# Kernel optimization log

Hardware: AMD Instinct MI355X
Metric: run time of the kernel (lower is better)

## Reference

```python
import jax, jax.numpy as jnp
import numpy as np

N = 50000      # num nodes
E = 1_600_000  # num edges (avg degree 32)
L = 200_000    # num label edges to decode
D_IN, H1, H2 = 256, 128, 64


def setup_inputs() -> dict:
    key = jax.random.key(0)
    ks = jax.random.split(key, 20)

    def w(k, fan_in, fan_out):
        return jax.random.normal(k, (fan_in, fan_out), jnp.float32) * (1.0 / np.sqrt(fan_in))

    return {
        'x': jax.random.normal(ks[0], (N, D_IN), jnp.float32),
        'prev0': jax.random.normal(ks[1], (N, H1), jnp.float32),
        'prev1': jax.random.normal(ks[2], (N, H2), jnp.float32),
        'Wpre1': w(ks[3], D_IN, 256), 'bpre1': jnp.zeros((256,), jnp.float32),
        'Wpre2': w(ks[4], 256, 128),  'bpre2': jnp.zeros((128,), jnp.float32),
        'Wc1': w(ks[5], 128, H1),     'bc1': jnp.zeros((H1,), jnp.float32),
        'Wc2': w(ks[6], H1, H2),      'bc2': jnp.zeros((H2,), jnp.float32),
        'Wm1': w(ks[7], 2 * H1, H1),  'bm1': jnp.zeros((H1,), jnp.float32),
        'Wm2': w(ks[8], 2 * H2, H2),  'bm2': jnp.zeros((H2,), jnp.float32),
        'Wpost': w(ks[9], H2, 2),     'bpost': jnp.zeros((2,), jnp.float32),
        'edge_index': jax.random.randint(ks[10], (2, E), 0, N, jnp.int32),
        'edge_label_index': jax.random.randint(ks[11], (2, L), 0, N, jnp.int32),
    }


def _gcn_conv(h, W, b, src, dst, n):
    """PyG GCNConv: add self-loops, sym-normalize D^-1/2 (A+I) D^-1/2 (X W) + b."""
    hw = h @ W                                   # [N, out]
    deg = jax.ops.segment_sum(jnp.ones_like(src, jnp.float32), dst, num_segments=n) + 1.0
    dinv = jax.lax.rsqrt(deg)                    # [N]
    norm = dinv[src] * dinv[dst]                 # [E]
    agg = jax.ops.segment_sum(hw[src] * norm[:, None], dst, num_segments=n)
    agg = agg + hw * (dinv * dinv)[:, None]      # self-loop term
    return agg + b


def reference(x, prev0, prev1, Wpre1, bpre1, Wpre2, bpre2, Wc1, bc1, Wc2, bc2,
              Wm1, bm1, Wm2, bm2, Wpost, bpost, edge_index, edge_label_index):
    # isnap > 0 with update='mlp'; dropout p=0.0 -> identity
    src, dst = edge_index[0], edge_index[1]
    n = x.shape[0]

    h = jax.nn.relu(x @ Wpre1 + bpre1)
    h = jax.nn.relu(h @ Wpre2 + bpre2)

    h = jax.nn.relu(_gcn_conv(h, Wc1, bc1, src, dst, n))
    h = jnp.concatenate([h, prev0], axis=1) @ Wm1 + bm1   # temporal MLP update 1
    emb0 = h

    h = jax.nn.relu(_gcn_conv(h, Wc2, bc2, src, dst, n))
    h = jnp.concatenate([h, prev1], axis=1) @ Wm2 + bm2   # temporal MLP update 2
    emb1 = h

    # hadamard edge decode
    h_had = emb1[edge_label_index[0]] * emb1[edge_label_index[1]]  # [L, H2]
    pred = jnp.sum(h_had @ Wpost + bpost, axis=-1)                 # [L]
    return pred, emb0, emb1
```

## Files before the change

### kernel.cpp

```cpp
#include <hip/hip_runtime.h>
#include <hip/hip_bf16.h>


typedef unsigned short ushort_t;
typedef __attribute__((ext_vector_type(8))) short s8v;
typedef __attribute__((ext_vector_type(4))) float f4;

#define BSHIFT 8

__device__ __forceinline__ ushort_t f2bf(float v) {
    unsigned u = __float_as_uint(v);
    return (ushort_t)((u + 0x7FFFu + ((u >> 16) & 1u)) >> 16);
}

__device__ __forceinline__ s8v cvt8(f4 v0, f4 v1) {
    ushort_t hb[8];
    hb[0] = f2bf(v0.x); hb[1] = f2bf(v0.y); hb[2] = f2bf(v0.z); hb[3] = f2bf(v0.w);
    hb[4] = f2bf(v1.x); hb[5] = f2bf(v1.y); hb[6] = f2bf(v1.z); hb[7] = f2bf(v1.w);
    return *(s8v*)hb;
}

__device__ __forceinline__ size_t swzidx(int row, int k, int Wd) {
    int p = (((k & 63) >> 3) ^ (row & 7));
    return (size_t)row * Wd + (k & ~63) + p * 8 + (k & 7);
}

__device__ __forceinline__ void dma16(const ushort_t* g, ushort_t* l) {
    __builtin_amdgcn_global_load_lds(
        (const __attribute__((address_space(1))) unsigned int*)g,
        (__attribute__((address_space(3))) unsigned int*)l, 16, 0, 0);
}

template <int W>
__global__ __launch_bounds__(256) void f2bswz_kernel(const float* __restrict__ in,
                                                     ushort_t* __restrict__ out, size_t n) {
    size_t i = ((size_t)blockIdx.x * 256 + threadIdx.x) * 8;
    if (i + 8 > n) return;
    f4 v0 = *(const f4*)&in[i];
    f4 v1 = *(const f4*)&in[i + 4];
    int row = (int)(i / W), k = (int)(i % W);
    *(s8v*)&out[swzidx(row, k, W)] = cvt8(v0, v1);
}

template <int BN, int KW, int K1, bool A1F32, bool RELU, bool SCALE, bool DUAL,
          int OUTMODE, bool SWZO>
__global__ __launch_bounds__(256, 2) void gemm_lds(
    const float* __restrict__ A1f, const ushort_t* __restrict__ A1h,
    const ushort_t* __restrict__ A2h,
    const ushort_t* __restrict__ Wt,
    const float* __restrict__ bias, const float* __restrict__ rowscale,
    float* __restrict__ Cf, ushort_t* __restrict__ Ch,
    int M, int Nout)
{
    constexpr int NT = BN / 32;
    constexpr int K2 = KW - K1;
    constexpr int NTILE = KW / 64;
    __shared__ ushort_t Abuf[2][128 * 64];
    __shared__ ushort_t Bbuf[2][BN * 64];

    const int tid  = threadIdx.x;
    const int lane = tid & 63;
    const int w    = tid >> 6;
    const int wr   = w >> 1, wc = w & 1;
    const int rbase = blockIdx.y * 128;
    const int bn    = blockIdx.x * BN;

    f4 acc[4][NT];
    const f4 zero = {0.f, 0.f, 0.f, 0.f};
#pragma unroll
    for (int mi = 0; mi < 4; ++mi)
#pragma unroll
        for (int ni = 0; ni < NT; ++ni) acc[mi][ni] = zero;

    f4 pr[8];

    auto gloadF32 = [&](int kt) {
#pragma unroll
        for (int j = 0; j < 4; ++j) {
            const int c2 = tid + j * 256;
            const int row = c2 >> 3, c = c2 & 7;
            const int gr = min(rbase + row, M - 1);
            const float* p = &A1f[(size_t)gr * K1 + kt + c * 8];
            pr[2 * j] = *(const f4*)p;
            pr[2 * j + 1] = *(const f4*)(p + 4);
        }
    };
    auto dswriteF32 = [&](int buf) {
#pragma unroll
        for (int j = 0; j < 4; ++j) {
            const int c2 = tid + j * 256;
            const int row = c2 >> 3, c = c2 & 7;
            const int pc = c ^ (row & 7);
            *(s8v*)&Abuf[buf][row * 64 + pc * 8] = cvt8(pr[2 * j], pr[2 * j + 1]);
        }
    };
    auto stageA = [&](int buf, int kt) {
#pragma unroll
        for (int i = 0; i < 4; ++i) {
            const int s = w * 4 + i;
            const int row = s * 8 + (lane >> 3);
            const int c = lane & 7;
            const int gr = min(rbase + row, M - 1);
            const ushort_t* g;
            if (DUAL && kt >= K1) g = &A2h[(size_t)gr * K2 + (kt - K1) + c * 8];
            else                  g = &A1h[(size_t)gr * K1 + kt + c * 8];
            dma16(g, &Abuf[buf][s * 512]);
        }
    };
    auto stageB = [&](int buf, int kt) {
#pragma unroll
        for (int i = 0; i < NT; ++i) {
            const int s = w * NT + i;
            const int colr = s * 8 + (lane >> 3);
            const int c = lane & 7;
            dma16(&Wt[(size_t)(bn + colr) * KW + kt + c * 8], &Bbuf[buf][s * 512]);
        }
    };

    if constexpr (A1F32) { gloadF32(0); dswriteF32(0); }
    else                 { stageA(0, 0); }
    stageB(0, 0);
    __syncthreads();

    for (int t = 0; t < NTILE; ++t) {
        const int cur = t & 1;
        if (t + 1 < NTILE) {
            if constexpr (A1F32) gloadF32((t + 1) * 64);
            else                 stageA(cur ^ 1, (t + 1) * 64);
            stageB(cur ^ 1, (t + 1) * 64);
        }
#pragma unroll
        for (int ks = 0; ks < 2; ++ks) {
            const int c = ks * 4 + (lane >> 4);
            s8v bfrag[NT];
#pragma unroll
            for (int ni = 0; ni < NT; ++ni) {
                const int colr = wc * (NT * 16) + ni * 16 + (lane & 15);
                bfrag[ni] = *(const s8v*)&Bbuf[cur][colr * 64 + (c ^ (colr & 7)) * 8];
            }
#pragma unroll
            for (int mi = 0; mi < 4; ++mi) {
                const int row = wr * 64 + mi * 16 + (lane & 15);
                const s8v af = *(const s8v*)&Abuf[cur][row * 64 + (c ^ (row & 7)) * 8];
#pragma unroll
                for (int ni = 0; ni < NT; ++ni)
                    acc[mi][ni] = __builtin_amdgcn_mfma_f32_16x16x32_bf16(af, bfrag[ni], acc[mi][ni], 0, 0, 0);
            }
        }
        if constexpr (A1F32) { if (t + 1 < NTILE) dswriteF32(cur ^ 1); }
        __syncthreads();
    }

#pragma unroll
    for (int mi = 0; mi < 4; ++mi) {
#pragma unroll
        for (int reg = 0; reg < 4; ++reg) {
            const int row = rbase + wr * 64 + mi * 16 + (lane >> 4) * 4 + reg;
            if (row >= M) continue;
            const float rs = SCALE ? rowscale[row] : 1.f;
#pragma unroll
            for (int ni = 0; ni < NT; ++ni) {
                const int col = bn + wc * (NT * 16) + ni * 16 + (lane & 15);
                float v = acc[mi][ni][reg];
                if (SCALE) v *= rs;
                if (bias) v += bias[col];
                if (RELU) v = fmaxf(v, 0.f);
                const size_t oidx = SWZO ? swzidx(row, col, Nout) : ((size_t)row * Nout + col);
                if constexpr (OUTMODE == 2) {
                    Ch[oidx] = f2bf(v);
                } else if constexpr (OUTMODE == 3) {
                    Cf[(size_t)row * Nout + col] = v;
                    Ch[oidx] = f2bf(v);
                } else {
                    Cf[(size_t)row * Nout + col] = v;
                }
            }
        }
    }
}

struct WDesc { const float* W; ushort_t* h; int K; int No; };
struct WAll { WDesc d[6]; };

__global__ void wtcvt_kernel(WAll wa) {
    WDesc d = wa.d[blockIdx.y];
    int e = blockIdx.x * blockDim.x + threadIdx.x;
    if (e >= d.K * d.No) return;
    int k = e / d.No, n = e - k * d.No;
    d.h[swzidx(n, k, d.K)] = f2bf(d.W[e]);
}

__global__ __launch_bounds__(256) void bcount_kernel(const int* __restrict__ dst,
                                                     int* __restrict__ bcount, int E, int NB) {
    __shared__ int cnt[256];
    const int t = threadIdx.x;
    if (t < NB) cnt[t] = 0;
    __syncthreads();
    for (int e = blockIdx.x * 256 + t; e < E; e += gridDim.x * 256)
        atomicAdd(&cnt[dst[e] >> BSHIFT], 1);
    __syncthreads();
    if (t < NB && cnt[t]) atomicAdd(&bcount[t], cnt[t]);
}

__global__ __launch_bounds__(256) void bscan_kernel(const int* __restrict__ bcount,
                                                    int* __restrict__ bbase,
                                                    int* __restrict__ bcursor, int NB, int E) {
    __shared__ int s[256];
    const int t = threadIdx.x;
    s[t] = (t < NB) ? bcount[t] : 0;
    __syncthreads();
    for (int off = 1; off < 256; off <<= 1) {
        int v = (t >= off) ? s[t - off] : 0;
        __syncthreads();
        s[t] += v;
        __syncthreads();
    }
    int excl = t ? s[t - 1] : 0;
    if (t < NB) { bbase[t] = excl; bcursor[t] = excl; }
    if (t == 0) bbase[NB] = E;
}

__global__ __launch_bounds__(256) void bpart_kernel(const int* __restrict__ src,
                                                    const int* __restrict__ dst,
                                                    int* __restrict__ bcursor,
                                                    unsigned* __restrict__ packed, int E, int NB) {
    __shared__ int cnt[256];
    __shared__ int cur[256];
    const int t = threadIdx.x;
    const int beg = blockIdx.x * 8192;
    const int end = min(beg + 8192, E);
    if (t < NB) cnt[t] = 0;
    __syncthreads();
    for (int e = beg + t; e < end; e += 256) atomicAdd(&cnt[dst[e] >> BSHIFT], 1);
    __syncthreads();
    if (t < NB && cnt[t]) cur[t] = atomicAdd(&bcursor[t], cnt[t]);
    __syncthreads();
    for (int e = beg + t; e < end; e += 256) {
        int d = dst[e];
        int b = d >> BSHIFT;
        int pos = atomicAdd(&cur[b], 1);
        packed[pos] = (unsigned)src[e] | ((unsigned)(d & ((1 << BSHIFT) - 1)) << 16);
    }
}

__global__ __launch_bounds__(256) void bbuild_kernel(const int* __restrict__ bbase,
                                                     const unsigned* __restrict__ packed,
                                                     int* __restrict__ col,
                                                     int* __restrict__ rowstart,
                                                     float* __restrict__ dinv, int N, int E) {
    __shared__ int ncnt[256];
    __shared__ int s[256];
    __shared__ int ncur[256];
    const int b = blockIdx.x;
    const int t = threadIdx.x;
    const int beg = bbase[b], end = bbase[b + 1];
    const int node0 = b << BSHIFT;
    const int nInB = min(256, N - node0);
    ncnt[t] = 0;
    __syncthreads();
    for (int e = beg + t; e < end; e += 256) atomicAdd(&ncnt[packed[e] >> 16], 1);
    __syncthreads();
    s[t] = ncnt[t];
    __syncthreads();
    for (int off = 1; off < 256; off <<= 1) {
        int v = (t >= off) ? s[t - off] : 0;
        __syncthreads();
        s[t] += v;
        __syncthreads();
    }
    int excl = t ? s[t - 1] : 0;
    if (t < nInB) {
        rowstart[node0 + t] = beg + excl;
        dinv[node0 + t] = rsqrtf((float)ncnt[t] + 1.0f);
    }
    ncur[t] = beg + excl;
    __syncthreads();
    for (int e = beg + t; e < end; e += 256) {
        unsigned p = packed[e];
        int pos = atomicAdd(&ncur[p >> 16], 1);
        col[pos] = (int)(p & 0xFFFFu);
    }
    if (b == 0 && t == 0) rowstart[N] = E;
}

template <int F>
__global__ __launch_bounds__(256) void gather_bf_kernel(const int* __restrict__ rowstart,
                                                        const int* __restrict__ col,
                                                        const float* __restrict__ dinv,
                                                        const ushort_t* __restrict__ hws,
                                                        const float* __restrict__ bias,
                                                        ushort_t* __restrict__ aggb, int N) {
    const int wave = threadIdx.x >> 6;
    const int lane = threadIdx.x & 63;
    const int d = blockIdx.x * 4 + wave;
    if (d >= N) return;
    const int beg = rowstart[d], end = rowstart[d + 1];
    const float dd = dinv[d];
    if (F == 128) {
        const unsigned* base = (const unsigned*)hws;
        unsigned sv = base[(size_t)d * 64 + lane];
        float ax = __uint_as_float(sv << 16);
        float ay = __uint_as_float(sv & 0xFFFF0000u);
        for (int e0 = beg; e0 < end; e0 += 64) {
            int nid = (e0 + lane < end) ? col[e0 + lane] : 0;
            int cnt = min(64, end - e0);
            int j = 0;
            for (; j + 8 <= cnt; j += 8) {
                unsigned u[8];
#pragma unroll
                for (int q = 0; q < 8; ++q) {
                    int s = __shfl(nid, j + q);
                    u[q] = base[(size_t)s * 64 + lane];
                }
#pragma unroll
                for (int q = 0; q < 8; ++q) {
                    ax += __uint_as_float(u[q] << 16);
                    ay += __uint_as_float(u[q] & 0xFFFF0000u);
                }
            }
            for (; j < cnt; ++j) {
                int s = __shfl(nid, j);
                unsigned uu = base[(size_t)s * 64 + lane];
                ax += __uint_as_float(uu << 16);
                ay += __uint_as_float(uu & 0xFFFF0000u);
            }
        }
        float2 b = ((const float2*)bias)[lane];
        float rx = fmaxf(ax * dd + b.x, 0.f);
        float ry = fmaxf(ay * dd + b.y, 0.f);
        unsigned pk = ((unsigned)f2bf(ry) << 16) | (unsigned)f2bf(rx);
        const int p = ((lane >> 2) & 7) ^ (d & 7);
        const int uidx = (lane >> 5) * 32 + p * 4 + (lane & 3);
        ((unsigned*)aggb)[(size_t)d * 64 + uidx] = pk;
    } else {
        float acc = __uint_as_float((unsigned)hws[(size_t)d * 64 + lane] << 16);
        for (int e0 = beg; e0 < end; e0 += 64) {
            int nid = (e0 + lane < end) ? col[e0 + lane] : 0;
            int cnt = min(64, end - e0);
            int j = 0;
            for (; j + 8 <= cnt; j += 8) {
                ushort_t u[8];
#pragma unroll
                for (int q = 0; q < 8; ++q) {
                    int s = __shfl(nid, j + q);
                    u[q] = hws[(size_t)s * 64 + lane];
                }
#pragma unroll
                for (int q = 0; q < 8; ++q) acc += __uint_as_float((unsigned)u[q] << 16);
            }
            for (; j < cnt; ++j) {
                int s = __shfl(nid, j);
                acc += __uint_as_float((unsigned)hws[(size_t)s * 64 + lane] << 16);
            }
        }
        acc = fmaxf(acc * dd + bias[lane], 0.f);
        const int p = (lane >> 3) ^ (d & 7);
        aggb[(size_t)d * 64 + p * 8 + (lane & 7)] = f2bf(acc);
    }
}

__global__ __launch_bounds__(256) void decode_kernel(const ushort_t* __restrict__ emb1b,
                                                     const int* __restrict__ eli,
                                                     const float* __restrict__ Wpost,
                                                     const float* __restrict__ bpost,
                                                     float* __restrict__ pred, int L) {
    const int wave = threadIdx.x >> 6;
    const int lane = threadIdx.x & 63;
    const int l = blockIdx.x * 4 + wave;
    if (l >= L) return;
    int s = eli[l];
    int d = eli[L + l];
    float w = Wpost[lane * 2] + Wpost[lane * 2 + 1];
    float a = __uint_as_float((unsigned)emb1b[(size_t)s * 64 + lane] << 16);
    float b = __uint_as_float((unsigned)emb1b[(size_t)d * 64 + lane] << 16);
    float p = a * b * w;
#pragma unroll
    for (int off = 32; off; off >>= 1) p += __shfl_down(p, off);
    if (lane == 0) pred[l] = p + bpost[0] + bpost[1];
}

extern "C" void kernel_launch(void* const* d_in, const int* in_sizes, int n_in,
                              void* d_out, int out_size, void* d_ws, size_t ws_size,
                              hipStream_t stream) {
    const float* x     = (const float*)d_in[0];
    const float* prev0 = (const float*)d_in[1];
    const float* prev1 = (const float*)d_in[2];
    const float* Wpre1 = (const float*)d_in[3];
    const float* bpre1 = (const float*)d_in[4];
    const float* Wpre2 = (const float*)d_in[5];
    const float* bpre2 = (const float*)d_in[6];
    const float* Wc1   = (const float*)d_in[7];
    const float* bc1   = (const float*)d_in[8];
    const float* Wc2   = (const float*)d_in[9];
    const float* bc2   = (const float*)d_in[10];
    const float* Wm1   = (const float*)d_in[11];
    const float* bm1   = (const float*)d_in[12];
    const float* Wm2   = (const float*)d_in[13];
    const float* bm2   = (const float*)d_in[14];
    const float* Wpost = (const float*)d_in[15];
    const float* bpost = (const float*)d_in[16];
    const int* edge_index = (const int*)d_in[17];
    const int* eli        = (const int*)d_in[18];

    const int N = in_sizes[0] / 256;
    const int E = in_sizes[17] / 2;
    const int L = in_sizes[18] / 2;
    const int NB = (N + 255) >> BSHIFT;

    const int* src = edge_index;
    const int* dst = edge_index + E;

    float* out  = (float*)d_out;
    float* pred = out;
    float* emb0 = out + L;
    float* emb1 = out + L + (size_t)N * 128;

    float* ws = (float*)d_ws;
    unsigned* packed = (unsigned*)ws;
    ushort_t* h1h   = (ushort_t*)ws;
    ushort_t* hws1b = (ushort_t*)ws;
    ushort_t* emb0b = (ushort_t*)ws;
    ushort_t* emb1b = (ushort_t*)ws;
    ushort_t* agg1b = (ushort_t*)(ws + (size_t)64 * N);
    ushort_t* hws2b = (ushort_t*)(ws + (size_t)64 * N);
    ushort_t* agg2b = (ushort_t*)(ws + (size_t)96 * N);
    ushort_t* h2b   = (ushort_t*)(ws + (size_t)128 * N);
    ushort_t* p0b   = (ushort_t*)(ws + (size_t)192 * N);
    ushort_t* p1b   = (ushort_t*)(ws + (size_t)256 * N);
    int*      col   = (int*)(ws + (size_t)288 * N);

    size_t o = (size_t)320 * N;
    int* rowstart = (int*)(ws + o);         o += ((size_t)N + 4) & ~(size_t)3;
    float* dinv = ws + o;                   o += ((size_t)N + 3) & ~(size_t)3;
    int* bbase = (int*)(ws + o);            o += 260;
    int* bcursor = (int*)(ws + o);          o += 260;
    int* bcount = (int*)(ws + o);           o += 260;
    ushort_t* wb = (ushort_t*)(ws + o);

    ushort_t* wpre1t = wb + 0;
    ushort_t* wpre2t = wb + 65536;
    ushort_t* wc1t   = wb + 98304;
    ushort_t* wm1t   = wb + 114688;
    ushort_t* wc2t   = wb + 147456;
    ushort_t* wm2t   = wb + 155648;

    {
        size_t n0 = (size_t)N * 128, n1 = (size_t)N * 64;
        f2bswz_kernel<128><<<(int)((n0 / 8 + 255) / 256), 256, 0, stream>>>(prev0, p0b, n0);
        f2bswz_kernel<64><<<(int)((n1 / 8 + 255) / 256), 256, 0, stream>>>(prev1, p1b, n1);
    }

    hipMemsetAsync(bcount, 0, (size_t)NB * sizeof(int), stream);
    bcount_kernel<<<1024, 256, 0, stream>>>(dst, bcount, E, NB);
    bscan_kernel<<<1, 256, 0, stream>>>(bcount, bbase, bcursor, NB, E);
    bpart_kernel<<<(E + 8191) / 8192, 256, 0, stream>>>(src, dst, bcursor, packed, E, NB);
    bbuild_kernel<<<NB, 256, 0, stream>>>(bbase, packed, col, rowstart, dinv, N, E);

    WAll wa;
    wa.d[0] = {Wpre1, wpre1t, 256, 256};
    wa.d[1] = {Wpre2, wpre2t, 256, 128};
    wa.d[2] = {Wc1,   wc1t,   128, 128};
    wa.d[3] = {Wm1,   wm1t,   256, 128};
    wa.d[4] = {Wc2,   wc2t,   128, 64};
    wa.d[5] = {Wm2,   wm2t,   128, 64};
    wtcvt_kernel<<<dim3(256, 6), 256, 0, stream>>>(wa);

    const int gy = (N + 127) / 128;

    gemm_lds<128, 256, 256, true, true, false, false, 2, true><<<dim3(2, gy), 256, 0, stream>>>(
        x, nullptr, nullptr, wpre1t, bpre1, nullptr, nullptr, h1h, N, 256);
    gemm_lds<128, 256, 256, false, true, false, false, 2, true><<<dim3(1, gy), 256, 0, stream>>>(
        nullptr, h1h, nullptr, wpre2t, bpre2, nullptr, nullptr, h2b, N, 128);
    gemm_lds<128, 128, 128, false, false, true, false, 2, false><<<dim3(1, gy), 256, 0, stream>>>(
        nullptr, h2b, nullptr, wc1t, nullptr, dinv, nullptr, hws1b, N, 128);
    gather_bf_kernel<128><<<(N + 3) / 4, 256, 0, stream>>>(rowstart, col, dinv, hws1b, bc1, agg1b, N);
    gemm_lds<128, 256, 128, false, false, false, true, 3, true><<<dim3(1, gy), 256, 0, stream>>>(
        nullptr, agg1b, p0b, wm1t, bm1, nullptr, emb0, emb0b, N, 128);
    gemm_lds<64, 128, 128, false, false, true, false, 2, false><<<dim3(1, gy), 256, 0, stream>>>(
        nullptr, emb0b, nullptr, wc2t, nullptr, dinv, nullptr, hws2b, N, 64);
    gather_bf_kernel<64><<<(N + 3) / 4, 256, 0, stream>>>(rowstart, col, dinv, hws2b, bc2, agg2b, N);
    gemm_lds<64, 128, 64, false, false, false, true, 3, false><<<dim3(1, gy), 256, 0, stream>>>(
        nullptr, agg2b, p1b, wm2t, bm2, nullptr, emb1, emb1b, N, 64);
    decode_kernel<<<(L + 3) / 4, 256, 0, stream>>>(emb1b, eli, Wpost, bpost, pred, L);
}
```

Before: 342.8 us.

## Replace double-buffered LDS pipeline with single-buffer load-sync-compute loop in GEMM

Removes double buffering and prefetch of the next K tile in the LDS GEMM. Each iteration now loads one A and B tile into a single shared buffer, syncs, computes, and syncs again. This halves LDS usage and register pressure, which may allow more resident blocks, but it stops global loads from overlapping with MFMA compute.

```diff
diff --git a/kernel.cpp b/kernel.cpp
--- a/kernel.cpp
+++ b/kernel.cpp
@@ -54,9 +54,8 @@
 {
     constexpr int NT = BN / 32;
     constexpr int K2 = KW - K1;
-    constexpr int NTILE = KW / 64;
-    __shared__ ushort_t Abuf[2][128 * 64];
-    __shared__ ushort_t Bbuf[2][BN * 64];
+    __shared__ ushort_t Abuf[128 * 64];
+    __shared__ ushort_t Bbuf[BN * 64];
 
     const int tid  = threadIdx.x;
     const int lane = tid & 63;
@@ -72,63 +71,38 @@
 #pragma unroll
         for (int ni = 0; ni < NT; ++ni) acc[mi][ni] = zero;
 
-    f4 pr[8];
-
-    auto gloadF32 = [&](int kt) {
-#pragma unroll
-        for (int j = 0; j < 4; ++j) {
-            const int c2 = tid + j * 256;
-            const int row = c2 >> 3, c = c2 & 7;
-            const int gr = min(rbase + row, M - 1);
-            const float* p = &A1f[(size_t)gr * K1 + kt + c * 8];
-            pr[2 * j] = *(const f4*)p;
-            pr[2 * j + 1] = *(const f4*)(p + 4);
-        }
-    };
-    auto dswriteF32 = [&](int buf) {
-#pragma unroll
-        for (int j = 0; j < 4; ++j) {
-            const int c2 = tid + j * 256;
-            const int row = c2 >> 3, c = c2 & 7;
-            const int pc = c ^ (row & 7);
-            *(s8v*)&Abuf[buf][row * 64 + pc * 8] = cvt8(pr[2 * j], pr[2 * j + 1]);
-        }
-    };
-    auto stageA = [&](int buf, int kt) {
-#pragma unroll
-        for (int i = 0; i < 4; ++i) {
-            const int s = w * 4 + i;
-            const int row = s * 8 + (lane >> 3);
-            const int c = lane & 7;
-            const int gr = min(rbase + row, M - 1);
-            const ushort_t* g;
-            if (DUAL && kt >= K1) g = &A2h[(size_t)gr * K2 + (kt - K1) + c * 8];
-            else                  g = &A1h[(size_t)gr * K1 + kt + c * 8];
-            dma16(g, &Abuf[buf][s * 512]);
-        }
-    };
-    auto stageB = [&](int buf, int kt) {
+    for (int kt = 0; kt < KW; kt += 64) {
+        if constexpr (A1F32) {
+#pragma unroll
+            for (int j = 0; j < 4; ++j) {
+                const int c2 = tid + j * 256;
+                const int row = c2 >> 3, c = c2 & 7;
+                const int gr = min(rbase + row, M - 1);
+                const float* p = &A1f[(size_t)gr * K1 + kt + c * 8];
+                const int pc = c ^ (row & 7);
+                *(s8v*)&Abuf[row * 64 + pc * 8] = cvt8(*(const f4*)p, *(const f4*)(p + 4));
+            }
+        } else {
+#pragma unroll
+            for (int i = 0; i < 4; ++i) {
+                const int s = w * 4 + i;
+                const int row = s * 8 + (lane >> 3);
+                const int c = lane & 7;
+                const int gr = min(rbase + row, M - 1);
+                const ushort_t* g;
+                if (DUAL && kt >= K1) g = &A2h[(size_t)gr * K2 + (kt - K1) + c * 8];
+                else                  g = &A1h[(size_t)gr * K1 + kt + c * 8];
+                dma16(g, &Abuf[s * 512]);
+            }
+        }
 #pragma unroll
         for (int i = 0; i < NT; ++i) {
             const int s = w * NT + i;
             const int colr = s * 8 + (lane >> 3);
             const int c = lane & 7;
-            dma16(&Wt[(size_t)(bn + colr) * KW + kt + c * 8], &Bbuf[buf][s * 512]);
-        }
-    };
-
-    if constexpr (A1F32) { gloadF32(0); dswriteF32(0); }
-    else                 { stageA(0, 0); }
-    stageB(0, 0);
-    __syncthreads();
-
-    for (int t = 0; t < NTILE; ++t) {
-        const int cur = t & 1;
-        if (t + 1 < NTILE) {
-            if constexpr (A1F32) gloadF32((t + 1) * 64);
-            else                 stageA(cur ^ 1, (t + 1) * 64);
-            stageB(cur ^ 1, (t + 1) * 64);
-        }
+            dma16(&Wt[(size_t)(bn + colr) * KW + kt + c * 8], &Bbuf[s * 512]);
+        }
+        __syncthreads();
 #pragma unroll
         for (int ks = 0; ks < 2; ++ks) {
             const int c = ks * 4 + (lane >> 4);
@@ -136,18 +110,17 @@
 #pragma unroll
             for (int ni = 0; ni < NT; ++ni) {
                 const int colr = wc * (NT * 16) + ni * 16 + (lane & 15);
-                bfrag[ni] = *(const s8v*)&Bbuf[cur][colr * 64 + (c ^ (colr & 7)) * 8];
+                bfrag[ni] = *(const s8v*)&Bbuf[colr * 64 + (c ^ (colr & 7)) * 8];
             }
 #pragma unroll
             for (int mi = 0; mi < 4; ++mi) {
                 const int row = wr * 64 + mi * 16 + (lane & 15);
-                const s8v af = *(const s8v*)&Abuf[cur][row * 64 + (c ^ (row & 7)) * 8];
+                const s8v af = *(const s8v*)&Abuf[row * 64 + (c ^ (row & 7)) * 8];
 #pragma unroll
                 for (int ni = 0; ni < NT; ++ni)
                     acc[mi][ni] = __builtin_amdgcn_mfma_f32_16x16x32_bf16(af, bfrag[ni], acc[mi][ni], 0, 0, 0);
             }
         }
-        if constexpr (A1F32) { if (t + 1 < NTILE) dswriteF32(cur ^ 1); }
         __syncthreads();
     }
 
```

After: 329.0 us. -4.0%, faster.
